# Performance work log

Measured on AMD Instinct MI355X. Metric: run time of the kernel, lower is better.

The kernel has to match this reference:

```python
import jax, jax.numpy as jnp
import numpy as np

B, T, D, H = 16, 1024, 2048, 512


def _lstm_dir(x, w_ih, w_hh, b_ih, b_hh, reverse):
    # x: (B,T,Din); w_ih: (4H,Din); w_hh: (4H,H). PyTorch gate order: i,f,g,o.
    h_dim = w_hh.shape[1]
    xg = jnp.einsum('btd,gd->btg', x, w_ih) + b_ih + b_hh  # (B,T,4H) input gates precomputed

    def step(carry, xg_t):
        h, c = carry
        g = xg_t + h @ w_hh.T
        i, f, gg, o = jnp.split(g, 4, axis=-1)
        i = jax.nn.sigmoid(i)
        f = jax.nn.sigmoid(f)
        gg = jnp.tanh(gg)
        o = jax.nn.sigmoid(o)
        c = f * c + i * gg
        h = o * jnp.tanh(c)
        return (h, c), h

    b = x.shape[0]
    init = (jnp.zeros((b, h_dim), x.dtype), jnp.zeros((b, h_dim), x.dtype))
    _, hs = jax.lax.scan(step, init, jnp.swapaxes(xg, 0, 1), reverse=reverse)
    return jnp.swapaxes(hs, 0, 1)  # (B,T,H)


def _bilstm_layer(x, p_fwd, p_bwd):
    out_f = _lstm_dir(x, *p_fwd, reverse=False)
    out_b = _lstm_dir(x, *p_bwd, reverse=True)
    return jnp.concatenate([out_f, out_b], axis=-1)  # (B,T,2H)


def setup_inputs() -> dict:
    key = jax.random.key(0)
    ks = jax.random.split(key, 20)
    s = 1.0 / np.sqrt(H)

    def u(k, shape):
        return jax.random.uniform(k, shape, jnp.float32, -s, s)

    inp = {'x': jax.random.normal(ks[0], (B, T, D), jnp.float32)}
    i = 1
    for layer, din in [(0, D), (1, 2 * H)]:
        for suf in ['', '_rev']:
            inp[f'w_ih_l{layer}{suf}'] = u(ks[i], (4 * H, din)); i += 1
            inp[f'w_hh_l{layer}{suf}'] = u(ks[i], (4 * H, H)); i += 1
            inp[f'b_ih_l{layer}{suf}'] = u(ks[i], (4 * H,)); i += 1
            inp[f'b_hh_l{layer}{suf}'] = u(ks[i], (4 * H,)); i += 1
            i -= 2  # reuse keys sparingly
            inp[f'b_ih_l{layer}{suf}'] = u(jax.random.fold_in(ks[i], 1), (4 * H,))
            inp[f'b_hh_l{layer}{suf}'] = u(jax.random.fold_in(ks[i], 2), (4 * H,))
            i += 2
    inp['attn_w'] = u(ks[17], (1, 2 * H))
    inp['attn_b'] = u(ks[18], (1,))
    return inp


def reference(x,
              w_ih_l0, w_hh_l0, b_ih_l0, b_hh_l0,
              w_ih_l0_rev, w_hh_l0_rev, b_ih_l0_rev, b_hh_l0_rev,
              w_ih_l1, w_hh_l1, b_ih_l1, b_hh_l1,
              w_ih_l1_rev, w_hh_l1_rev, b_ih_l1_rev, b_hh_l1_rev,
              attn_w, attn_b):
    out = _bilstm_layer(x,
                        (w_ih_l0, w_hh_l0, b_ih_l0, b_hh_l0),
                        (w_ih_l0_rev, w_hh_l0_rev, b_ih_l0_rev, b_hh_l0_rev))
    out = _bilstm_layer(out,
                        (w_ih_l1, w_hh_l1, b_ih_l1, b_hh_l1),
                        (w_ih_l1_rev, w_hh_l1_rev, b_ih_l1_rev, b_hh_l1_rev))
    # attention pooling: Linear(2H -> 1), softmax over time, weighted sum
    scores = jnp.einsum('bth,oh->bto', out, attn_w) + attn_b  # (B,T,1)
    weights = jax.nn.softmax(scores, axis=1)
    encoding = jnp.sum(weights * out, axis=1)  # (B, 2H)
    return encoding
```

## Files before the change

### kernel.cpp

```cpp
#include <hip/hip_runtime.h>
#include <hip/hip_bf16.h>
#include <cstdio>

typedef unsigned short ushort_t;
typedef unsigned long long u64;
typedef __attribute__((ext_vector_type(4))) float f32x4;
typedef __attribute__((ext_vector_type(4))) unsigned int u32x4;
typedef __attribute__((ext_vector_type(8))) __bf16 bf16x8;
typedef __attribute__((ext_vector_type(8))) unsigned short u16x8;
typedef __attribute__((ext_vector_type(4))) unsigned short u16x4;

#define B_  16
#define T_  1024
#define H_  512
#define NG  2048
#define M_  (B_*T_)
#define NBLK_DIR 16
#define FLG_STRIDE 64

__device__ inline unsigned short f2bf_rne(float f){
  union { float f; unsigned int u; } v; v.f = f;
  unsigned int u = v.u;
  unsigned int r = (u + 0x7fffu + ((u >> 16) & 1u)) >> 16;
  return (unsigned short)r;
}
__device__ inline float bf2f(unsigned short s){
  union { unsigned int u; float f; } v; v.u = ((unsigned int)s) << 16;
  return v.f;
}
__device__ inline float sigm_f(float x){
  return 1.0f / (1.0f + __expf(-x));
}
__device__ inline float tanh_f(float x){
  return 1.0f - 2.0f / (__expf(2.0f * x) + 1.0f);
}

__global__ void zero_u32(unsigned* __restrict__ p, int n){
  int i = blockIdx.x * blockDim.x + threadIdx.x;
  if (i < n) p[i] = 0u;
}

__global__ void split_f32_bf16(const float* __restrict__ src,
                               ushort_t* __restrict__ hi, ushort_t* __restrict__ lo,
                               int n4){
  int i = blockIdx.x * blockDim.x + threadIdx.x;
  int stride = gridDim.x * blockDim.x;
  for (; i < n4; i += stride){
    f32x4 v = ((const f32x4*)src)[i];
    u16x4 h4, l4;
    #pragma unroll
    for (int j = 0; j < 4; j++){
      unsigned short h = f2bf_rne(v[j]);
      h4[j] = h;
      l4[j] = f2bf_rne(v[j] - bf2f(h));
    }
    ((u16x4*)hi)[i] = h4;
    ((u16x4*)lo)[i] = l4;
  }
}

__global__ __launch_bounds__(256) void gemm_xg(
    const ushort_t* __restrict__ Ahi, const ushort_t* __restrict__ Alo,
    const ushort_t* __restrict__ Bhi0, const ushort_t* __restrict__ Blo0,
    const ushort_t* __restrict__ Bhi1, const ushort_t* __restrict__ Blo1,
    const float* __restrict__ bi0, const float* __restrict__ bh0,
    const float* __restrict__ bi1, const float* __restrict__ bh1,
    float* __restrict__ C0, float* __restrict__ C1,
    int M, int N, int K)
{
  __shared__ ushort_t As[128*32];
  __shared__ ushort_t Bs[128*32];
  const int tid  = threadIdx.x;
  const int wave = tid >> 6, lane = tid & 63;
  const int l15 = lane & 15, l4 = lane >> 4;
  const int wr = wave >> 1, wc = wave & 1;
  const int n0 = blockIdx.x * 128, m0 = blockIdx.y * 128;
  const int dir = blockIdx.z;
  const ushort_t* Bhi = dir ? Bhi1 : Bhi0;
  const ushort_t* Blo = dir ? Blo1 : Blo0;
  const float* bia = dir ? bi1 : bi0;
  const float* bib = dir ? bh1 : bh0;
  float* C = dir ? C1 : C0;

  f32x4 acc[4][4];
  #pragma unroll
  for (int i = 0; i < 4; i++)
    #pragma unroll
    for (int j = 0; j < 4; j++) acc[i][j] = (f32x4){0.f,0.f,0.f,0.f};

  const int e0 = tid, e1 = 256 + tid;
  const int row0 = e0 >> 2, c80 = (e0 & 3) * 8;
  const int row1 = e1 >> 2, c81 = (e1 & 3) * 8;

  for (int seg = 0; seg < 3; ++seg){
    const ushort_t* Ap = (seg == 2) ? Alo : Ahi;
    const ushort_t* Bp = (seg == 1) ? Blo : Bhi;
    for (int kt = 0; kt < K; kt += 32){
      __builtin_amdgcn_global_load_lds(
        (const __attribute__((address_space(1))) unsigned int*)(Ap + (size_t)(m0 + row0) * K + kt + c80),
        (__attribute__((address_space(3))) unsigned int*)(As + e0 * 8), 16, 0, 0);
      __builtin_amdgcn_global_load_lds(
        (const __attribute__((address_space(1))) unsigned int*)(Bp + (size_t)(n0 + row0) * K + kt + c80),
        (__attribute__((address_space(3))) unsigned int*)(Bs + e0 * 8), 16, 0, 0);
      __builtin_amdgcn_global_load_lds(
        (const __attribute__((address_space(1))) unsigned int*)(Ap + (size_t)(m0 + row1) * K + kt + c81),
        (__attribute__((address_space(3))) unsigned int*)(As + e1 * 8), 16, 0, 0);
      __builtin_amdgcn_global_load_lds(
        (const __attribute__((address_space(1))) unsigned int*)(Bp + (size_t)(n0 + row1) * K + kt + c81),
        (__attribute__((address_space(3))) unsigned int*)(Bs + e1 * 8), 16, 0, 0);
      __syncthreads();
      bf16x8 af[4], bfr[4];
      #pragma unroll
      for (int m = 0; m < 4; m++)
        af[m] = *(const bf16x8*)(As + (wr*64 + m*16 + l15) * 32 + l4 * 8);
      #pragma unroll
      for (int n = 0; n < 4; n++)
        bfr[n] = *(const bf16x8*)(Bs + (wc*64 + n*16 + l15) * 32 + l4 * 8);
      #pragma unroll
      for (int m = 0; m < 4; m++)
        #pragma unroll
        for (int n = 0; n < 4; n++)
          acc[m][n] = __builtin_amdgcn_mfma_f32_16x16x32_bf16(af[m], bfr[n], acc[m][n], 0, 0, 0);
      __syncthreads();
    }
  }
  #pragma unroll
  for (int m = 0; m < 4; m++)
    #pragma unroll
    for (int n = 0; n < 4; n++){
      int col = n0 + wc*64 + n*16 + l15;
      float bias = bia[col] + bib[col];
      #pragma unroll
      for (int r = 0; r < 4; r++){
        int row = m0 + wr*64 + m*16 + l4*4 + r;
        C[(size_t)row * N + col] = acc[m][n][r] + bias;
      }
    }
}

__global__ __launch_bounds__(512, 1) void lstm_layer(
    const float* __restrict__ whh_fwd, const float* __restrict__ whh_bwd,
    const float* __restrict__ xg,
    unsigned* __restrict__ hbuf,
    unsigned* __restrict__ flags,
    float* __restrict__ out_f32,
    ushort_t* __restrict__ out_hi,
    ushort_t* __restrict__ out_lo)
{
  const int dir = blockIdx.x >> 4;
  const int cb  = blockIdx.x & 15;
  const int tid = threadIdx.x;
  const int wave = tid >> 6, lane = tid & 63;
  const int gate = wave >> 1, ch = wave & 1;
  const int l15 = lane & 15, l4 = lane >> 4;
  const float* whh = dir ? whh_bwd : whh_fwd;
  unsigned* hb = hbuf + (size_t)dir * 2 * 8192;
  unsigned* flg = flags + (size_t)dir * FLG_STRIDE;

  __shared__ ushort_t hfhi[8192];
  __shared__ ushort_t hflo[8192];
  __shared__ float gbuf[4][16][33];
  __shared__ unsigned s_token;

  bf16x8 Whi[16], Wlo[16];
  {
    const int wrow = gate * 512 + cb * 32 + ch * 16 + l15;
    const float* p0 = whh + (size_t)wrow * 512;
    #pragma unroll
    for (int s = 0; s < 16; s++){
      const float* p = p0 + s * 32 + l4 * 8;
      f32x4 va = *(const f32x4*)(p);
      f32x4 vb = *(const f32x4*)(p + 4);
      u16x8 th, tl;
      #pragma unroll
      for (int j = 0; j < 4; j++){
        unsigned short h = f2bf_rne(va[j]);
        th[j] = h; tl[j] = f2bf_rne(va[j] - bf2f(h));
        unsigned short h2 = f2bf_rne(vb[j]);
        th[4+j] = h2; tl[4+j] = f2bf_rne(vb[j] - bf2f(h2));
      }
      Whi[s] = __builtin_bit_cast(bf16x8, th);
      Wlo[s] = __builtin_bit_cast(bf16x8, tl);
    }
  }

  const int eb = tid >> 5, ecl = tid & 31, ecol = cb * 32 + ecl;

  const int p   = tid >> 5;
  const int b5  = tid & 31;
  const int cb_b  = b5 >> 1;
  const int lo1 = b5 & 1;
  const int unitBase = (p * 4 + lo1 * 2) * 16 + cb_b;

  if (tid == 0) s_token = 0u;
  __hip_atomic_store(&hb[cb * 512 + tid], 0u, __ATOMIC_RELAXED, __HIP_MEMORY_SCOPE_AGENT);
  __syncthreads();
  if (tid == 0)
    __hip_atomic_store(&flg[cb], 1u, __ATOMIC_RELAXED, __HIP_MEMORY_SCOPE_AGENT);

  float c_state = 0.0f;

  for (int t = 0; t < T_; ++t){
    const int t_eff = dir ? (T_ - 1 - t) : t;
    const float* xgp = xg + ((size_t)dir * M_ + (size_t)eb * T_ + t_eff) * NG + ecol;
    float xi = xgp[0];
    float xf = xgp[512];
    float xgg = xgp[1024];
    float xo = xgp[1536];

    const unsigned want = (unsigned)(t + 1);
    if (wave == 0){
      if (lane < NBLK_DIR){
        while (__hip_atomic_load(&flg[lane], __ATOMIC_RELAXED, __HIP_MEMORY_SCOPE_AGENT) < want)
          __builtin_amdgcn_s_sleep(1);
      }
      if (lane == 0)
        __hip_atomic_store(&s_token, want, __ATOMIC_RELEASE, __HIP_MEMORY_SCOPE_WORKGROUP);
    } else {
      while (__hip_atomic_load(&s_token, __ATOMIC_ACQUIRE, __HIP_MEMORY_SCOPE_WORKGROUP) < want)
        __builtin_amdgcn_s_sleep(1);
    }

    const u64* src = (const u64*)(hb + (size_t)(t & 1) * 8192) + (size_t)p * 256 + (size_t)b5 * 8;
    u64 v[8];
    #pragma unroll
    for (int k = 0; k < 8; k++)
      v[k] = __hip_atomic_load(&src[k], __ATOMIC_RELAXED, __HIP_MEMORY_SCOPE_AGENT);

    {
      u32x4 wh0, wh1, wl0, wl1;
      #pragma unroll
      for (int k = 0; k < 4; k++){
        unsigned d0 = (unsigned)v[k], d1 = (unsigned)(v[k] >> 32);
        wh0[k] = (d0 & 0xffffu) | (d1 << 16);
        wl0[k] = (d0 >> 16) | (d1 & 0xffff0000u);
      }
      #pragma unroll
      for (int k = 0; k < 4; k++){
        unsigned d0 = (unsigned)v[4 + k], d1 = (unsigned)(v[4 + k] >> 32);
        wh1[k] = (d0 & 0xffffu) | (d1 << 16);
        wl1[k] = (d0 >> 16) | (d1 & 0xffff0000u);
      }
      ((u32x4*)hfhi)[unitBase]      = wh0;
      ((u32x4*)hfhi)[unitBase + 16] = wh1;
      ((u32x4*)hflo)[unitBase]      = wl0;
      ((u32x4*)hflo)[unitBase + 16] = wl1;
    }
    __syncthreads();

    {
      f32x4 a0 = {0.f,0.f,0.f,0.f}, a1 = a0, a2 = a0;
      #pragma unroll
      for (int s = 0; s < 16; s++){
        bf16x8 ah = *(const bf16x8*)&hfhi[(s * 64 + l4 * 16 + l15) * 8];
        bf16x8 al = *(const bf16x8*)&hflo[(s * 64 + l4 * 16 + l15) * 8];
        a0 = __builtin_amdgcn_mfma_f32_16x16x32_bf16(ah, Whi[s], a0, 0, 0, 0);
        a1 = __builtin_amdgcn_mfma_f32_16x16x32_bf16(ah, Wlo[s], a1, 0, 0, 0);
        a2 = __builtin_amdgcn_mfma_f32_16x16x32_bf16(al, Whi[s], a2, 0, 0, 0);
      }
      f32x4 acc = a0 + a1;
      acc = acc + a2;
      #pragma unroll
      for (int r = 0; r < 4; r++)
        gbuf[gate][l4 * 4 + r][ch * 16 + l15] = acc[r];
    }
    __syncthreads();

    float h; unsigned short hh, hl; size_t oidx;
    {
      float pi = gbuf[0][eb][ecl] + xi;
      float pf = gbuf[1][eb][ecl] + xf;
      float pg = gbuf[2][eb][ecl] + xgg;
      float po = gbuf[3][eb][ecl] + xo;
      float ig = sigm_f(pi);
      float fg = sigm_f(pf);
      float gg = tanh_f(pg);
      float og = sigm_f(po);
      c_state = fg * c_state + ig * gg;
      h = og * tanh_f(c_state);
      hh = f2bf_rne(h);
      hl = f2bf_rne(h - bf2f(hh));
      oidx = ((size_t)eb * T_ + t_eff) * 1024 + dir * 512 + ecol;
      __hip_atomic_store(&hb[(size_t)((t + 1) & 1) * 8192 + cb * 512 + tid],
                         (unsigned)hh | ((unsigned)hl << 16),
                         __ATOMIC_RELAXED, __HIP_MEMORY_SCOPE_AGENT);
    }
    __syncthreads();
    if (tid == 0)
      __hip_atomic_store(&flg[cb], (unsigned)(t + 2), __ATOMIC_RELAXED, __HIP_MEMORY_SCOPE_AGENT);
    if (out_f32) out_f32[oidx] = h;
    if (out_hi){ out_hi[oidx] = hh; out_lo[oidx] = hl; }
  }
}

__device__ inline float dot4(f32x4 a, f32x4 b){
  return a[0]*b[0] + a[1]*b[1] + a[2]*b[2] + a[3]*b[3];
}

__global__ __launch_bounds__(256) void attn_pool(
    const float* __restrict__ out1,
    const float* __restrict__ aw,
    const float* __restrict__ ab,
    float* __restrict__ enc)
{
  __shared__ float wbuf[1024];
  __shared__ float sc[1024];
  __shared__ float red[16];
  const int b = blockIdx.x;
  const int tid = threadIdx.x;
  const int wave = tid >> 6, lane = tid & 63;
  ((f32x4*)wbuf)[tid] = ((const f32x4*)aw)[tid];
  __syncthreads();
  const float* ob = out1 + (size_t)b * T_ * 1024;
  const float bias = ab[0];

  for (int t = wave; t < T_; t += 4){
    const float* row = ob + (size_t)t * 1024;
    float s = dot4(((const f32x4*)row)[lane],       ((const f32x4*)wbuf)[lane])
            + dot4(((const f32x4*)row)[lane + 64],  ((const f32x4*)wbuf)[lane + 64])
            + dot4(((const f32x4*)row)[lane + 128], ((const f32x4*)wbuf)[lane + 128])
            + dot4(((const f32x4*)row)[lane + 192], ((const f32x4*)wbuf)[lane + 192]);
    #pragma unroll
    for (int o = 32; o > 0; o >>= 1) s += __shfl_xor(s, o, 64);
    if (lane == 0) sc[t] = s + bias;
  }
  __syncthreads();

  float m = -1e30f;
  for (int i = tid; i < 1024; i += 256) m = fmaxf(m, sc[i]);
  #pragma unroll
  for (int o = 32; o > 0; o >>= 1) m = fmaxf(m, __shfl_xor(m, o, 64));
  if (lane == 0) red[wave] = m;
  __syncthreads();
  m = fmaxf(fmaxf(red[0], red[1]), fmaxf(red[2], red[3]));

  float ssum = 0.f;
  for (int i = tid; i < 1024; i += 256){
    float p = __expf(sc[i] - m);
    sc[i] = p;
    ssum += p;
  }
  #pragma unroll
  for (int o = 32; o > 0; o >>= 1) ssum += __shfl_xor(ssum, o, 64);
  if (lane == 0) red[8 + wave] = ssum;
  __syncthreads();
  float inv = 1.0f / (red[8] + red[9] + red[10] + red[11]);

  f32x4 a = {0.f,0.f,0.f,0.f};
  for (int t = 0; t < T_; t++){
    f32x4 v = *(const f32x4*)(ob + (size_t)t * 1024 + tid * 4);
    float p = sc[t];
    a[0] += p * v[0]; a[1] += p * v[1]; a[2] += p * v[2]; a[3] += p * v[3];
  }
  f32x4 r = { a[0]*inv, a[1]*inv, a[2]*inv, a[3]*inv };
  *(f32x4*)(enc + (size_t)b * 1024 + tid * 4) = r;
}

extern "C" void kernel_launch(void* const* d_in, const int* in_sizes, int n_in,
                              void* d_out, int out_size, void* d_ws, size_t ws_size,
                              hipStream_t stream)
{
  const float* x        = (const float*)d_in[0];
  const float* w_ih_l0  = (const float*)d_in[1];
  const float* w_hh_l0  = (const float*)d_in[2];
  const float* b_ih_l0  = (const float*)d_in[3];
  const float* b_hh_l0  = (const float*)d_in[4];
  const float* w_ih_l0r = (const float*)d_in[5];
  const float* w_hh_l0r = (const float*)d_in[6];
  const float* b_ih_l0r = (const float*)d_in[7];
  const float* b_hh_l0r = (const float*)d_in[8];
  const float* w_ih_l1  = (const float*)d_in[9];
  const float* w_hh_l1  = (const float*)d_in[10];
  const float* b_ih_l1  = (const float*)d_in[11];
  const float* b_hh_l1  = (const float*)d_in[12];
  const float* w_ih_l1r = (const float*)d_in[13];
  const float* w_hh_l1r = (const float*)d_in[14];
  const float* b_ih_l1r = (const float*)d_in[15];
  const float* b_hh_l1r = (const float*)d_in[16];
  const float* attn_w   = (const float*)d_in[17];
  const float* attn_b   = (const float*)d_in[18];
  float* enc = (float*)d_out;

  char* ws = (char*)d_ws;
  size_t off = 0;
  auto alloc = [&](size_t bytes) -> void* {
    void* p = ws + off;
    off += (bytes + 255) & ~(size_t)255;
    return p;
  };
  ushort_t* Ahi  = (ushort_t*)alloc((size_t)M_ * 2048 * 2);
  ushort_t* Alo  = (ushort_t*)alloc((size_t)M_ * 2048 * 2);
  ushort_t* Whi0 = (ushort_t*)alloc((size_t)2048 * 2048 * 2);
  ushort_t* Wlo0 = (ushort_t*)alloc((size_t)2048 * 2048 * 2);
  ushort_t* Whi1 = (ushort_t*)alloc((size_t)2048 * 2048 * 2);
  ushort_t* Wlo1 = (ushort_t*)alloc((size_t)2048 * 2048 * 2);
  float*    xg   = (float*)alloc((size_t)2 * M_ * NG * 4);
  float*    outb = (float*)alloc((size_t)M_ * 1024 * 4);
  unsigned* hbuf = (unsigned*)alloc((size_t)2 * 2 * 2 * 8192 * 4);
  unsigned* flags= (unsigned*)alloc((size_t)2 * 2 * FLG_STRIDE * 4);
  if (off > ws_size){
    fprintf(stderr, "kernel_launch: workspace too small: need %zu have %zu\n", off, ws_size);
    return;
  }

  {
    int n = 2 * 2 * 2 * 8192 + 2 * 2 * FLG_STRIDE;
    zero_u32<<<(n + 255) / 256, 256, 0, stream>>>(hbuf, n);
  }

  split_f32_bf16<<<2048, 256, 0, stream>>>(x, Ahi, Alo, M_ * 2048 / 4);
  split_f32_bf16<<<512, 256, 0, stream>>>(w_ih_l0,  Whi0, Wlo0, 2048 * 2048 / 4);
  split_f32_bf16<<<512, 256, 0, stream>>>(w_ih_l0r, Whi1, Wlo1, 2048 * 2048 / 4);
  gemm_xg<<<dim3(16, 128, 2), 256, 0, stream>>>(
      Ahi, Alo, Whi0, Wlo0, Whi1, Wlo1,
      b_ih_l0, b_hh_l0, b_ih_l0r, b_hh_l0r,
      xg, xg + (size_t)M_ * NG, M_, NG, 2048);
  lstm_layer<<<32, 512, 0, stream>>>(w_hh_l0, w_hh_l0r, xg, hbuf, flags,
                                     nullptr, Ahi, Alo);
  split_f32_bf16<<<512, 256, 0, stream>>>(w_ih_l1,  Whi0, Wlo0, 2048 * 1024 / 4);
  split_f32_bf16<<<512, 256, 0, stream>>>(w_ih_l1r, Whi1, Wlo1, 2048 * 1024 / 4);
  gemm_xg<<<dim3(16, 128, 2), 256, 0, stream>>>(
      Ahi, Alo, Whi0, Wlo0, Whi1, Wlo1,
      b_ih_l1, b_hh_l1, b_ih_l1r, b_hh_l1r,
      xg, xg + (size_t)M_ * NG, M_, NG, 1024);
  lstm_layer<<<32, 512, 0, stream>>>(w_hh_l1, w_hh_l1r, xg,
                                     hbuf + (size_t)2 * 2 * 8192,
                                     flags + (size_t)2 * FLG_STRIDE,
                                     outb, nullptr, nullptr);
  attn_pool<<<16, 256, 0, stream>>>(outb, attn_w, attn_b, enc);
}
```

Measured before the change: 10.32 ms.

## Replicate per-block step flags and fold layer-1 weight split into LSTM launch

Each recurrent block now writes its step counter into a 16x16 flag matrix, one copy per reader, so every block polls its own row instead of all blocks polling the same 16 flags. This spreads the polling traffic across separate addresses at the cost of 16 stores per step. The layer-0 recurrent kernel is also launched with extra blocks that do the fp32-to-bf16 hi/lo split of the layer-1 input weights. That removes two separate launches and overlaps the split with the latency-bound recurrence, at the risk of the extra blocks competing for memory bandwidth with it.

```diff
diff --git a/kernel.cpp b/kernel.cpp
--- a/kernel.cpp
+++ b/kernel.cpp
@@ -16,7 +16,7 @@
 #define NG  2048
 #define M_  (B_*T_)
 #define NBLK_DIR 16
-#define FLG_STRIDE 64
+#define FLG_DIR  256
 
 __device__ inline unsigned short f2bf_rne(float f){
   union { float f; unsigned int u; } v; v.f = f;
@@ -40,12 +40,10 @@
   if (i < n) p[i] = 0u;
 }
 
-__global__ void split_f32_bf16(const float* __restrict__ src,
-                               ushort_t* __restrict__ hi, ushort_t* __restrict__ lo,
-                               int n4){
-  int i = blockIdx.x * blockDim.x + threadIdx.x;
-  int stride = gridDim.x * blockDim.x;
-  for (; i < n4; i += stride){
+__device__ inline void split_range(const float* __restrict__ src,
+                                   ushort_t* __restrict__ hi, ushort_t* __restrict__ lo,
+                                   int n4, int idx, int stride){
+  for (int i = idx; i < n4; i += stride){
     f32x4 v = ((const f32x4*)src)[i];
     u16x4 h4, l4;
     #pragma unroll
@@ -57,6 +55,13 @@
     ((u16x4*)hi)[i] = h4;
     ((u16x4*)lo)[i] = l4;
   }
+}
+
+__global__ void split_f32_bf16(const float* __restrict__ src,
+                               ushort_t* __restrict__ hi, ushort_t* __restrict__ lo,
+                               int n4){
+  split_range(src, hi, lo, n4,
+              blockIdx.x * blockDim.x + threadIdx.x, gridDim.x * blockDim.x);
 }
 
 __global__ __launch_bounds__(256) void gemm_xg(
@@ -145,17 +150,30 @@
     unsigned* __restrict__ flags,
     float* __restrict__ out_f32,
     ushort_t* __restrict__ out_hi,
-    ushort_t* __restrict__ out_lo)
+    ushort_t* __restrict__ out_lo,
+    const float* __restrict__ spl_src0, ushort_t* __restrict__ spl_hi0,
+    ushort_t* __restrict__ spl_lo0, int spl_n0,
+    const float* __restrict__ spl_src1, ushort_t* __restrict__ spl_hi1,
+    ushort_t* __restrict__ spl_lo1, int spl_n1)
 {
+  const int tid = threadIdx.x;
+
+  if (blockIdx.x >= 2 * NBLK_DIR){
+    const int idx = (blockIdx.x - 2 * NBLK_DIR) * 512 + tid;
+    const int stride = (gridDim.x - 2 * NBLK_DIR) * 512;
+    if (spl_src0) split_range(spl_src0, spl_hi0, spl_lo0, spl_n0, idx, stride);
+    if (spl_src1) split_range(spl_src1, spl_hi1, spl_lo1, spl_n1, idx, stride);
+    return;
+  }
+
   const int dir = blockIdx.x >> 4;
   const int cb  = blockIdx.x & 15;
-  const int tid = threadIdx.x;
   const int wave = tid >> 6, lane = tid & 63;
   const int gate = wave >> 1, ch = wave & 1;
   const int l15 = lane & 15, l4 = lane >> 4;
   const float* whh = dir ? whh_bwd : whh_fwd;
   unsigned* hb = hbuf + (size_t)dir * 2 * 8192;
-  unsigned* flg = flags + (size_t)dir * FLG_STRIDE;
+  unsigned* flg = flags + (size_t)dir * FLG_DIR;
 
   __shared__ ushort_t hfhi[8192];
   __shared__ ushort_t hflo[8192];
@@ -195,8 +213,8 @@
   if (tid == 0) s_token = 0u;
   __hip_atomic_store(&hb[cb * 512 + tid], 0u, __ATOMIC_RELAXED, __HIP_MEMORY_SCOPE_AGENT);
   __syncthreads();
-  if (tid == 0)
-    __hip_atomic_store(&flg[cb], 1u, __ATOMIC_RELAXED, __HIP_MEMORY_SCOPE_AGENT);
+  if (tid < NBLK_DIR)
+    __hip_atomic_store(&flg[tid * NBLK_DIR + cb], 1u, __ATOMIC_RELAXED, __HIP_MEMORY_SCOPE_AGENT);
 
   float c_state = 0.0f;
 
@@ -211,7 +229,8 @@
     const unsigned want = (unsigned)(t + 1);
     if (wave == 0){
       if (lane < NBLK_DIR){
-        while (__hip_atomic_load(&flg[lane], __ATOMIC_RELAXED, __HIP_MEMORY_SCOPE_AGENT) < want)
+        const unsigned* f = &flg[cb * NBLK_DIR + lane];
+        while (__hip_atomic_load(f, __ATOMIC_RELAXED, __HIP_MEMORY_SCOPE_AGENT) < want)
           __builtin_amdgcn_s_sleep(1);
       }
       if (lane == 0)
@@ -286,8 +305,9 @@
                          __ATOMIC_RELAXED, __HIP_MEMORY_SCOPE_AGENT);
     }
     __syncthreads();
-    if (tid == 0)
-      __hip_atomic_store(&flg[cb], (unsigned)(t + 2), __ATOMIC_RELAXED, __HIP_MEMORY_SCOPE_AGENT);
+    if (tid < NBLK_DIR)
+      __hip_atomic_store(&flg[tid * NBLK_DIR + cb], (unsigned)(t + 2),
+                         __ATOMIC_RELAXED, __HIP_MEMORY_SCOPE_AGENT);
     if (out_f32) out_f32[oidx] = h;
     if (out_hi){ out_hi[oidx] = hh; out_lo[oidx] = hl; }
   }
@@ -397,14 +417,14 @@
   float*    xg   = (float*)alloc((size_t)2 * M_ * NG * 4);
   float*    outb = (float*)alloc((size_t)M_ * 1024 * 4);
   unsigned* hbuf = (unsigned*)alloc((size_t)2 * 2 * 2 * 8192 * 4);
-  unsigned* flags= (unsigned*)alloc((size_t)2 * 2 * FLG_STRIDE * 4);
+  unsigned* flags= (unsigned*)alloc((size_t)2 * 2 * FLG_DIR * 4);
   if (off > ws_size){
     fprintf(stderr, "kernel_launch: workspace too small: need %zu have %zu\n", off, ws_size);
     return;
   }
 
   {
-    int n = 2 * 2 * 2 * 8192 + 2 * 2 * FLG_STRIDE;
+    int n = 2 * 2 * 2 * 8192 + 2 * 2 * FLG_DIR;
     zero_u32<<<(n + 255) / 256, 256, 0, stream>>>(hbuf, n);
   }
 
@@ -415,17 +435,19 @@
       Ahi, Alo, Whi0, Wlo0, Whi1, Wlo1,
       b_ih_l0, b_hh_l0, b_ih_l0r, b_hh_l0r,
       xg, xg + (size_t)M_ * NG, M_, NG, 2048);
-  lstm_layer<<<32, 512, 0, stream>>>(w_hh_l0, w_hh_l0r, xg, hbuf, flags,
-                                     nullptr, Ahi, Alo);
-  split_f32_bf16<<<512, 256, 0, stream>>>(w_ih_l1,  Whi0, Wlo0, 2048 * 1024 / 4);
-  split_f32_bf16<<<512, 256, 0, stream>>>(w_ih_l1r, Whi1, Wlo1, 2048 * 1024 / 4);
+  lstm_layer<<<256, 512, 0, stream>>>(w_hh_l0, w_hh_l0r, xg, hbuf, flags,
+                                      nullptr, Ahi, Alo,
+                                      w_ih_l1,  Whi0, Wlo0, 2048 * 1024 / 4,
+                                      w_ih_l1r, Whi1, Wlo1, 2048 * 1024 / 4);
   gemm_xg<<<dim3(16, 128, 2), 256, 0, stream>>>(
       Ahi, Alo, Whi0, Wlo0, Whi1, Wlo1,
       b_ih_l1, b_hh_l1, b_ih_l1r, b_hh_l1r,
       xg, xg + (size_t)M_ * NG, M_, NG, 1024);
   lstm_layer<<<32, 512, 0, stream>>>(w_hh_l1, w_hh_l1r, xg,
                                      hbuf + (size_t)2 * 2 * 8192,
-                                     flags + (size_t)2 * FLG_STRIDE,
-                                     outb, nullptr, nullptr);
+                                     flags + (size_t)2 * FLG_DIR,
+                                     outb, nullptr, nullptr,
+                                     nullptr, nullptr, nullptr, 0,
+                                     nullptr, nullptr, nullptr, 0);
   attn_pool<<<16, 256, 0, stream>>>(outb, attn_w, attn_b, enc);
 }
```

Measured after the change: 10.07 ms (median of 2 runs). 2.4% less time.
